# Performance work log

Hardware: AMD Instinct MI355X
Metric: run time of the kernel (lower is better)

Reference implementation:

```python
import jax, jax.numpy as jnp
import numpy as np
from jax import lax

S = 2          # scale_factor
K = 5          # k_reassembly
KK = K * K     # 25 reassembly weights per output pixel


def _conv2d(x, w, b, pad):
    y = lax.conv_general_dilated(x, w, (1, 1), [(pad, pad), (pad, pad)],
                                 dimension_numbers=('NCHW', 'OIHW', 'NCHW'))
    return y + b[None, :, None, None]


def _pixel_shuffle(x, r):
    # (N, C*r*r, H, W) -> (N, C, H*r, W*r), torch PixelShuffle semantics
    n, crr, h, w = x.shape
    c = crr // (r * r)
    x = x.reshape(n, c, r, r, h, w)
    x = x.transpose(0, 1, 4, 2, 5, 3)
    return x.reshape(n, c, h * r, w * r)


def setup_inputs() -> dict:
    key = jax.random.key(0)
    k1, k2, k3 = jax.random.split(key, 3)
    x = jax.random.normal(k1, (4, 256, 64, 64), dtype=jnp.float32)
    w_comp = jax.random.normal(k2, (64, 256, 1, 1), dtype=jnp.float32) * 0.05
    b_comp = jnp.zeros((64,), dtype=jnp.float32)
    w_enc = jax.random.normal(k3, (S * S * KK, 64, 3, 3), dtype=jnp.float32) * 0.05
    b_enc = jnp.zeros((S * S * KK,), dtype=jnp.float32)
    return {"x": x, "w_comp": w_comp, "b_comp": b_comp, "w_enc": w_enc, "b_enc": b_enc}


def reference(x, w_comp, b_comp, w_enc, b_enc):
    N, C, H, W = x.shape
    p = K // 2
    # kernel prediction branch
    compressed = _conv2d(x, w_comp, b_comp, pad=0)                 # (N, 64, H, W)
    kernels = _conv2d(compressed, w_enc, b_enc, pad=1)             # (N, S*S*KK, H, W)
    kernels = _pixel_shuffle(kernels, S)                           # (N, KK, H*S, W*S)
    kernels = jax.nn.softmax(kernels, axis=1)
    # regroup kernels: (N, KK, Hs, Ws) -> (N, H, W, KK, S*S)  (torch unfold order: kh then kw)
    k_unf = kernels.reshape(N, KK, H, S, W, S)
    k_unf = k_unf.transpose(0, 2, 4, 1, 3, 5).reshape(N, H, W, KK, S * S)
    # gather KxK input patches: (N, C, H, W, KK), flattened (ih, iw) with ih outer
    xp = jnp.pad(x, ((0, 0), (0, 0), (p, p), (p, p)))
    patches = jnp.stack([xp[:, :, i:i + H, j:j + W]
                         for i in range(K) for j in range(K)], axis=-1)
    # weighted reassembly: per-pixel (C, KK) @ (KK, S*S)
    out = jnp.einsum('nchwk,nhwkq->nhwcq', patches, k_unf)          # (N, H, W, C, S*S)
    out = out.reshape(N, H, W, C * S * S).transpose(0, 3, 1, 2)     # (N, C*S*S, H, W)
    return _pixel_shuffle(out, S)                                   # (N, C, H*S, W*S)
```

## Files before the change

### kernel.cpp

```cpp
#include <hip/hip_runtime.h>
#include <hip/hip_fp16.h>

#define NB 4
#define CI 256
#define HH 64
#define WW 64
#define MC 64
#define HS 128
#define WS_ 128
#define HW 4096

typedef __attribute__((ext_vector_type(8))) short short8v;
typedef __attribute__((ext_vector_type(4))) float floatx4;

__device__ inline unsigned short f2bf(float f) {
  union { float f; unsigned u; } v; v.f = f;
  unsigned r = v.u + 0x7FFFu + ((v.u >> 16) & 1u);
  return (unsigned short)(r >> 16);
}

__global__ __launch_bounds__(256) void prep_kernel(
    const float* __restrict__ w_comp, const float* __restrict__ w_enc,
    unsigned short* __restrict__ Aw1, unsigned short* __restrict__ Aw2) {
  int i = blockIdx.x * 256 + threadIdx.x;
  if (i < 16384) {
    int kl = i & 31, o = (i >> 5) & 63, ks = i >> 11;
    Aw1[i] = f2bf(w_comp[o * 256 + ks * 32 + kl]);
  } else if (i < 16384 + 64512) {
    int j = i - 16384;
    int kl = j & 31, o = (j >> 5) % 112, ks = (j >> 5) / 112;
    int t = ks >> 1, m = (ks & 1) * 32 + kl;
    Aw2[j] = (o < 100) ? f2bf(w_enc[o * 576 + m * 9 + t]) : (unsigned short)0;
  }
}

__global__ __launch_bounds__(512, 1) void conv1x1_mfma(
    const float* __restrict__ x, const unsigned short* __restrict__ Aw1,
    const float* __restrict__ b_comp, unsigned short* __restrict__ comp_cl) {
  __shared__ float pacc[2][64][49];
  int tid = threadIdx.x;
  int wid = tid >> 6, lane = tid & 63;
  int tileid = wid & 1, kh = wid >> 1;
  int Nt = blockIdx.x * 2 + tileid;
  int n = Nt >> 8, pixbase = (Nt & 255) * 16;
  int l15 = lane & 15, g = lane >> 4;
  int pix = pixbase + l15;

  floatx4 acc[4];
#pragma unroll
  for (int ot = 0; ot < 4; ++ot) acc[ot] = (floatx4){0.f, 0.f, 0.f, 0.f};

  const float* xb = x + (size_t)n * CI * HW + pix;
  const unsigned short* ab = Aw1 + l15 * 32 + g * 8;

#pragma unroll
  for (int s = 0; s < 2; ++s) {
    int ks = kh * 2 + s;
    int c0 = ks * 32 + g * 8;
    short8v bfrag;
#pragma unroll
    for (int j = 0; j < 8; ++j)
      bfrag[j] = (short)f2bf(xb[(size_t)(c0 + j) * HW]);
#pragma unroll
    for (int ot = 0; ot < 4; ++ot) {
      short8v af = *(const short8v*)(ab + (ks * 64 + ot * 16) * 32);
      acc[ot] = __builtin_amdgcn_mfma_f32_16x16x32_bf16(af, bfrag, acc[ot], 0, 0, 0);
    }
  }

  if (kh > 0) {
#pragma unroll
    for (int ot = 0; ot < 4; ++ot)
#pragma unroll
      for (int r = 0; r < 4; ++r)
        pacc[tileid][lane][(kh - 1) * 16 + ot * 4 + r] = acc[ot][r];
  }
  __syncthreads();
  if (kh == 0) {
    unsigned short* cp = comp_cl + ((size_t)(n * HW + pix)) * 64;
#pragma unroll
    for (int ot = 0; ot < 4; ++ot) {
      const float4 bv = *(const float4*)(b_comp + ot * 16 + g * 4);
      float v0 = acc[ot][0] + bv.x, v1 = acc[ot][1] + bv.y;
      float v2 = acc[ot][2] + bv.z, v3 = acc[ot][3] + bv.w;
#pragma unroll
      for (int sl = 0; sl < 3; ++sl) {
        v0 += pacc[tileid][lane][sl * 16 + ot * 4 + 0];
        v1 += pacc[tileid][lane][sl * 16 + ot * 4 + 1];
        v2 += pacc[tileid][lane][sl * 16 + ot * 4 + 2];
        v3 += pacc[tileid][lane][sl * 16 + ot * 4 + 3];
      }
      unsigned h01 = (unsigned)f2bf(v0) | ((unsigned)f2bf(v1) << 16);
      unsigned h23 = (unsigned)f2bf(v2) | ((unsigned)f2bf(v3) << 16);
      *(int2*)(cp + ot * 16 + g * 4) = make_int2((int)h01, (int)h23);
    }
  }
}

#define PKLO(W, D, ACC)                                                        \
  asm("v_pk_fma_f16 %0, %1, %2, %0 op_sel:[0,0,0] op_sel_hi:[1,0,1]"           \
      : "+v"(ACC) : "v"(W), "v"(D));
#define PKHI(W, D, ACC)                                                        \
  asm("v_pk_fma_f16 %0, %1, %2, %0 op_sel:[0,1,0] op_sel_hi:[1,1,1]"           \
      : "+v"(ACC) : "v"(W), "v"(D));

#define ROWPK(WA, WB, WC, WD, WE, VA, VB, VC, VD, VE, RP)                      \
  { const unsigned* rr = (const unsigned*)(RP);                                \
    unsigned d0 = rr[0], d1 = rr[1], d2 = rr[2];                               \
    PKLO(WA, d0, aA) PKHI(WB, d0, aA) PKLO(WC, d1, aA)                         \
    PKHI(WD, d1, aA) PKLO(WE, d2, aA)                                          \
    PKHI(VA, d0, aB) PKLO(VB, d1, aB) PKHI(VC, d1, aB)                         \
    PKLO(VD, d2, aB) PKHI(VE, d2, aB) }

__device__ __forceinline__ float4 load_slot20(const float* __restrict__ xb,
                                              int h0, int w0, int f,
                                              bool interior) {
  int c = f / 30, rem = f - c * 30, r = rem / 5, h = rem - r * 5;
  int gh = h0 - 2 + r, gw = w0 - 2 + h * 4;
  if (interior) {
    const float* gp = xb + (size_t)c * HW + gh * WW + gw;
    float2 lo = *(const float2*)gp;
    float2 hi = *(const float2*)(gp + 2);
    return make_float4(lo.x, lo.y, hi.x, hi.y);
  }
  int ghc = min(max(gh, 0), 63);
  const float* rowp = xb + (size_t)c * HW + ghc * WW;
  float v0 = rowp[min(max(gw + 0, 0), 63)];
  float v1 = rowp[min(max(gw + 1, 0), 63)];
  float v2 = rowp[min(max(gw + 2, 0), 63)];
  float v3 = rowp[min(max(gw + 3, 0), 63)];
  bool rok = ((unsigned)gh < 64u);
  v0 = (rok && (unsigned)(gw + 0) < 64u) ? v0 : 0.f;
  v1 = (rok && (unsigned)(gw + 1) < 64u) ? v1 : 0.f;
  v2 = (rok && (unsigned)(gw + 2) < 64u) ? v2 : 0.f;
  v3 = (rok && (unsigned)(gw + 3) < 64u) ? v3 : 0.f;
  return make_float4(v0, v1, v2, v3);
}

__device__ __forceinline__ uint2 f4_to_h4(float4 s) {
  __half2 a = __floats2half2_rn(s.x, s.y);
  __half2 b = __floats2half2_rn(s.z, s.w);
  return make_uint2(*(unsigned*)&a, *(unsigned*)&b);
}

__global__ __launch_bounds__(512, 4) void fused_kernel(
    const float* __restrict__ x,
    const unsigned short* __restrict__ comp_cl,
    const unsigned short* __restrict__ Aw2,
    const float* __restrict__ b_enc,
    float* __restrict__ out) {
  __shared__ float smem[12672];
  float* paccF = smem;
  unsigned short* xph = (unsigned short*)smem;
  unsigned int* wlds = (unsigned int*)(smem + 10880);

  int tid = threadIdx.x;
  int bid = blockIdx.x;
  int tile = bid & 127, n = bid >> 7;
  int tyi = tile >> 2, txi = tile & 3;
  int ty0 = tyi * 4, tx0 = txi * 32;
  int h0 = tyi * 2, w0 = txi * 16;

  int wid = tid >> 6, lane = tid & 63;
  int tileid = wid & 1, kh = wid >> 1;
  int l15 = lane & 15, g = lane >> 4;

  bool interior = (tyi >= 1) && (tyi <= 30) && (txi >= 1) && (txi <= 2);
  bool extra = tid < 448;

  const float* xb0g = x + (size_t)(n * CI) * HW;
  float4 pre0f = load_slot20(xb0g, h0, w0, tid, interior);
  float4 pre1f = extra ? load_slot20(xb0g, h0, w0, tid + 512, interior)
                       : make_float4(0.f, 0.f, 0.f, 0.f);

  {
    int pix = (h0 + tileid) * 64 + w0 + l15;
    int y = pix >> 6, xcol = pix & 63;

    bool vm[9];
    int sh9[9];
#pragma unroll
    for (int t = 0; t < 9; ++t) {
      int dy = t / 3, dx = t % 3;
      vm[t] = ((unsigned)(y + dy - 1) < 64u) && ((unsigned)(xcol + dx - 1) < 64u);
      sh9[t] = (dy - 1) * 64 + (dx - 1);
    }

    floatx4 acc[7];
#pragma unroll
    for (int ot = 0; ot < 7; ++ot) acc[ot] = (floatx4){0.f, 0.f, 0.f, 0.f};

    const unsigned short* cb = comp_cl + (size_t)n * HW * 64;
    const unsigned short* ab = Aw2 + l15 * 32 + g * 8;
    const short8v zv = {0, 0, 0, 0, 0, 0, 0, 0};

    int ks0 = (kh < 2) ? kh * 5 : 10 + (kh - 2) * 4;
    int len = (kh < 2) ? 5 : 4;

    short8v bf[5];
#pragma unroll
    for (int s = 0; s < 5; ++s) {
      int ks = ks0 + s; if (ks > 17) ks = 17;
      int t = ks >> 1, mh = ks & 1;
      const unsigned short* bp = cb + (pix + sh9[t]) * 64 + mh * 32 + g * 8;
      bf[s] = vm[t] ? *(const short8v*)bp : zv;
    }

#pragma unroll
    for (int s = 0; s < 5; ++s) {
      if (s < len) {
        int ks = ks0 + s;
#pragma unroll
        for (int ot = 0; ot < 7; ++ot) {
          short8v af = *(const short8v*)(ab + (ks * 112 + ot * 16) * 32);
          acc[ot] = __builtin_amdgcn_mfma_f32_16x16x32_bf16(af, bf[s], acc[ot], 0, 0, 0);
        }
      }
    }

    if (kh > 0) {
#pragma unroll
      for (int ot = 0; ot < 7; ++ot)
#pragma unroll
        for (int r = 0; r < 4; ++r)
          paccF[(tileid * 64 + lane) * 85 + (kh - 1) * 28 + ot * 4 + r] =
              acc[ot][r];
    }
    __syncthreads();
    if (kh == 0) {
#pragma unroll
      for (int ot = 0; ot < 7; ++ot) {
        int ob = ot * 16 + g * 4; if (ob > 96) ob = 96;
        const float4 bv = *(const float4*)(b_enc + ob);
        acc[ot][0] += bv.x; acc[ot][1] += bv.y;
        acc[ot][2] += bv.z; acc[ot][3] += bv.w;
#pragma unroll
        for (int sl = 0; sl < 3; ++sl) {
          acc[ot][0] += paccF[(tileid * 64 + lane) * 85 + sl * 28 + ot * 4 + 0];
          acc[ot][1] += paccF[(tileid * 64 + lane) * 85 + sl * 28 + ot * 4 + 1];
          acc[ot][2] += paccF[(tileid * 64 + lane) * 85 + sl * 28 + ot * 4 + 2];
          acc[ot][3] += paccF[(tileid * 64 + lane) * 85 + sl * 28 + ot * 4 + 3];
        }
      }

#pragma unroll
      for (int r = 0; r < 4; ++r) {
        float m = acc[0][r];
#pragma unroll
        for (int ot = 1; ot < 6; ++ot) m = fmaxf(m, acc[ot][r]);
        if (g == 0) m = fmaxf(m, acc[6][r]);
        m = fmaxf(m, __shfl_xor(m, 16));
        m = fmaxf(m, __shfl_xor(m, 32));
        float s = 0.f;
        float e[7];
#pragma unroll
        for (int ot = 0; ot < 7; ++ot) {
          bool val = (ot < 6) || (g == 0);
          e[ot] = val ? __expf(acc[ot][r] - m) : 0.f;
          s += e[ot];
        }
        s += __shfl_xor(s, 16);
        s += __shfl_xor(s, 32);
        float inv = 1.f / s;
#pragma unroll
        for (int ot = 0; ot < 7; ++ot) acc[ot][r] = e[ot] * inv;
      }

#pragma unroll
      for (int sh = 0; sh < 2; ++sh) {
        unsigned int* wq = wlds + sh * 896 + tileid * 448 + l15 * 28;
#pragma unroll
        for (int ot = 0; ot < 7; ++ot) {
          if ((ot < 6) || (g == 0)) {
            __half2 h2 = __floats2half2_rn(acc[ot][2 * sh], acc[ot][2 * sh + 1]);
            wq[ot * 4 + g] = *reinterpret_cast<unsigned int*>(&h2);
          }
        }
      }
    }
  }
  __syncthreads();

  int cslot = tid >> 5;
  int rem = tid & 31;
  int py = rem >> 4;
  int shsel = (rem >> 3) & 1;
  int pxp = rem & 7;
  int oy = ty0 + 2 * py + shsel;
  int ox0 = tx0 + 4 * pxp;
  int cb0 = 2 * pxp;

  const unsigned int* wtA = wlds + shsel * 896 + py * 448 + cb0 * 28;
  const unsigned int* wtB = wtA + 28;
  uint4 A0 = *(const uint4*)(wtA + 0);
  uint4 A1 = *(const uint4*)(wtA + 4);
  uint4 A2 = *(const uint4*)(wtA + 8);
  uint4 A3 = *(const uint4*)(wtA + 12);
  uint4 A4 = *(const uint4*)(wtA + 16);
  uint4 A5 = *(const uint4*)(wtA + 20);
  unsigned int A6 = wtA[24];
  uint4 B0 = *(const uint4*)(wtB + 0);
  uint4 B1 = *(const uint4*)(wtB + 4);
  uint4 B2 = *(const uint4*)(wtB + 8);
  uint4 B3 = *(const uint4*)(wtB + 12);
  uint4 B4 = *(const uint4*)(wtB + 16);
  uint4 B5 = *(const uint4*)(wtB + 20);
  unsigned int B6 = wtB[24];

  {
    uint2 p0 = f4_to_h4(pre0f);
    *(uint2*)(xph + 4 * tid) = p0;
    if (extra) {
      uint2 p1 = f4_to_h4(pre1f);
      *(uint2*)(xph + 4 * (tid + 512)) = p1;
    }
  }
  __syncthreads();

  for (int cs = 0; cs < 8; ++cs) {
    unsigned short* xpcur = xph + (cs & 1) * 3840;
    unsigned short* xpnxt = xph + ((cs + 1) & 1) * 3840;

    uint2 t0 = make_uint2(0u, 0u), t1 = make_uint2(0u, 0u);
    if (cs < 7) {
      const float* xbn = x + (size_t)(n * CI + (cs + 1) * 32) * HW;
      t0 = f4_to_h4(load_slot20(xbn, h0, w0, tid, interior));
      if (extra) t1 = f4_to_h4(load_slot20(xbn, h0, w0, tid + 512, interior));
    }

    float* outb = out + ((size_t)(n * CI + cs * 32) * HS + oy) * WS_ + ox0;
#pragma unroll
    for (int it = 0; it < 2; ++it) {
      int cl = it * 16 + cslot;
      const unsigned short* p = xpcur + cl * 120 + py * 20 + cb0;
      unsigned aA = 0u, aB = 0u;
      ROWPK(A0.x, A0.y, A0.z, A0.w, A1.x, B0.x, B0.y, B0.z, B0.w, B1.x, p)
      ROWPK(A1.y, A1.z, A1.w, A2.x, A2.y, B1.y, B1.z, B1.w, B2.x, B2.y, p + 20)
      ROWPK(A2.z, A2.w, A3.x, A3.y, A3.z, B2.z, B2.w, B3.x, B3.y, B3.z, p + 40)
      ROWPK(A3.w, A4.x, A4.y, A4.z, A4.w, B3.w, B4.x, B4.y, B4.z, B4.w, p + 60)
      ROWPK(A5.x, A5.y, A5.z, A5.w, A6,   B5.x, B5.y, B5.z, B5.w, B6,   p + 80)
      __half2 hA = *reinterpret_cast<__half2*>(&aA);
      __half2 hB = *reinterpret_cast<__half2*>(&aB);
      float2 fA = __half22float2(hA);
      float2 fB = __half22float2(hB);
      *(float4*)(outb + (size_t)cl * HS * WS_) =
          make_float4(fA.x, fA.y, fB.x, fB.y);
    }

    if (cs < 7) {
      *(uint2*)(xpnxt + 4 * tid) = t0;
      if (extra) *(uint2*)(xpnxt + 4 * (tid + 512)) = t1;
      __syncthreads();
    }
  }
}

extern "C" void kernel_launch(void* const* d_in, const int* in_sizes, int n_in,
                              void* d_out, int out_size, void* d_ws,
                              size_t ws_size, hipStream_t stream) {
  const float* x      = (const float*)d_in[0];
  const float* w_comp = (const float*)d_in[1];
  const float* b_comp = (const float*)d_in[2];
  const float* w_enc  = (const float*)d_in[3];
  const float* b_enc  = (const float*)d_in[4];
  float* out = (float*)d_out;

  char* ws = (char*)d_ws;
  unsigned short* comp_cl = (unsigned short*)ws;
  unsigned short* Aw1     = (unsigned short*)(ws + 2097152);
  unsigned short* Aw2     = (unsigned short*)(ws + 2129920);

  prep_kernel<<<dim3(316), 256, 0, stream>>>(w_comp, w_enc, Aw1, Aw2);
  conv1x1_mfma<<<dim3(512), 512, 0, stream>>>(x, Aw1, b_comp, comp_cl);
  fused_kernel<<<dim3(512), 512, 0, stream>>>(x, comp_cl, Aw2, b_enc, out);
}
```

Measured before the change: 54.04 us.

## Widen halo to 16B-aligned float4 loads and deepen x prefetch to triple buffer

```diff
diff --git a/kernel.cpp b/kernel.cpp
--- a/kernel.cpp
+++ b/kernel.cpp
@@ -112,16 +112,13 @@
     PKHI(VA, d0, aB) PKLO(VB, d1, aB) PKHI(VC, d1, aB)                         \
     PKLO(VD, d2, aB) PKHI(VE, d2, aB) }
 
-__device__ __forceinline__ float4 load_slot20(const float* __restrict__ xb,
+__device__ __forceinline__ float4 load_slot24(const float* __restrict__ xb,
                                               int h0, int w0, int f,
                                               bool interior) {
-  int c = f / 30, rem = f - c * 30, r = rem / 5, h = rem - r * 5;
-  int gh = h0 - 2 + r, gw = w0 - 2 + h * 4;
+  int c = f / 36, rem = f - c * 36, r = rem / 6, h = rem - r * 6;
+  int gh = h0 - 2 + r, gw = w0 - 4 + h * 4;
   if (interior) {
-    const float* gp = xb + (size_t)c * HW + gh * WW + gw;
-    float2 lo = *(const float2*)gp;
-    float2 hi = *(const float2*)(gp + 2);
-    return make_float4(lo.x, lo.y, hi.x, hi.y);
+    return *(const float4*)(xb + (size_t)c * HW + gh * WW + gw);
   }
   int ghc = min(max(gh, 0), 63);
   const float* rowp = xb + (size_t)c * HW + ghc * WW;
@@ -166,11 +163,12 @@
   int l15 = lane & 15, g = lane >> 4;
 
   bool interior = (tyi >= 1) && (tyi <= 30) && (txi >= 1) && (txi <= 2);
-  bool extra = tid < 448;
+  bool extra3 = tid < 128;
 
   const float* xb0g = x + (size_t)(n * CI) * HW;
-  float4 pre0f = load_slot20(xb0g, h0, w0, tid, interior);
-  float4 pre1f = extra ? load_slot20(xb0g, h0, w0, tid + 512, interior)
+  float4 preA = load_slot24(xb0g, h0, w0, tid, interior);
+  float4 preB = load_slot24(xb0g, h0, w0, tid + 512, interior);
+  float4 preC = extra3 ? load_slot24(xb0g, h0, w0, tid + 1024, interior)
                        : make_float4(0.f, 0.f, 0.f, 0.f);
 
   {
@@ -307,38 +305,44 @@
   uint4 B5 = *(const uint4*)(wtB + 20);
   unsigned int B6 = wtB[24];
 
+  *(uint2*)(xph + 4 * tid) = f4_to_h4(preA);
+  *(uint2*)(xph + 4 * (tid + 512)) = f4_to_h4(preB);
+  if (extra3) *(uint2*)(xph + 4 * (tid + 1024)) = f4_to_h4(preC);
+
+  float4 wA, wB, wC;
   {
-    uint2 p0 = f4_to_h4(pre0f);
-    *(uint2*)(xph + 4 * tid) = p0;
-    if (extra) {
-      uint2 p1 = f4_to_h4(pre1f);
-      *(uint2*)(xph + 4 * (tid + 512)) = p1;
-    }
+    const float* xb1 = x + (size_t)(n * CI + 32) * HW;
+    wA = load_slot24(xb1, h0, w0, tid, interior);
+    wB = load_slot24(xb1, h0, w0, tid + 512, interior);
+    wC = extra3 ? load_slot24(xb1, h0, w0, tid + 1024, interior)
+                : make_float4(0.f, 0.f, 0.f, 0.f);
   }
   __syncthreads();
 
   for (int cs = 0; cs < 8; ++cs) {
-    unsigned short* xpcur = xph + (cs & 1) * 3840;
-    unsigned short* xpnxt = xph + ((cs + 1) & 1) * 3840;
-
-    uint2 t0 = make_uint2(0u, 0u), t1 = make_uint2(0u, 0u);
-    if (cs < 7) {
-      const float* xbn = x + (size_t)(n * CI + (cs + 1) * 32) * HW;
-      t0 = f4_to_h4(load_slot20(xbn, h0, w0, tid, interior));
-      if (extra) t1 = f4_to_h4(load_slot20(xbn, h0, w0, tid + 512, interior));
+    unsigned short* xpcur = xph + (cs % 3) * 4608;
+    unsigned short* xpnxt = xph + ((cs + 1) % 3) * 4608;
+
+    float4 lA = make_float4(0.f, 0.f, 0.f, 0.f);
+    float4 lB = lA, lC = lA;
+    if (cs < 6) {
+      const float* xbn = x + (size_t)(n * CI + (cs + 2) * 32) * HW;
+      lA = load_slot24(xbn, h0, w0, tid, interior);
+      lB = load_slot24(xbn, h0, w0, tid + 512, interior);
+      if (extra3) lC = load_slot24(xbn, h0, w0, tid + 1024, interior);
     }
 
     float* outb = out + ((size_t)(n * CI + cs * 32) * HS + oy) * WS_ + ox0;
 #pragma unroll
     for (int it = 0; it < 2; ++it) {
       int cl = it * 16 + cslot;
-      const unsigned short* p = xpcur + cl * 120 + py * 20 + cb0;
+      const unsigned short* p = xpcur + cl * 144 + py * 24 + cb0 + 2;
       unsigned aA = 0u, aB = 0u;
       ROWPK(A0.x, A0.y, A0.z, A0.w, A1.x, B0.x, B0.y, B0.z, B0.w, B1.x, p)
-      ROWPK(A1.y, A1.z, A1.w, A2.x, A2.y, B1.y, B1.z, B1.w, B2.x, B2.y, p + 20)
-      ROWPK(A2.z, A2.w, A3.x, A3.y, A3.z, B2.z, B2.w, B3.x, B3.y, B3.z, p + 40)
-      ROWPK(A3.w, A4.x, A4.y, A4.z, A4.w, B3.w, B4.x, B4.y, B4.z, B4.w, p + 60)
-      ROWPK(A5.x, A5.y, A5.z, A5.w, A6,   B5.x, B5.y, B5.z, B5.w, B6,   p + 80)
+      ROWPK(A1.y, A1.z, A1.w, A2.x, A2.y, B1.y, B1.z, B1.w, B2.x, B2.y, p + 24)
+      ROWPK(A2.z, A2.w, A3.x, A3.y, A3.z, B2.z, B2.w, B3.x, B3.y, B3.z, p + 48)
+      ROWPK(A3.w, A4.x, A4.y, A4.z, A4.w, B3.w, B4.x, B4.y, B4.z, B4.w, p + 72)
+      ROWPK(A5.x, A5.y, A5.z, A5.w, A6,   B5.x, B5.y, B5.z, B5.w, B6,   p + 96)
       __half2 hA = *reinterpret_cast<__half2*>(&aA);
       __half2 hB = *reinterpret_cast<__half2*>(&aB);
       float2 fA = __half22float2(hA);
@@ -348,10 +352,12 @@
     }
 
     if (cs < 7) {
-      *(uint2*)(xpnxt + 4 * tid) = t0;
-      if (extra) *(uint2*)(xpnxt + 4 * (tid + 512)) = t1;
+      *(uint2*)(xpnxt + 4 * tid) = f4_to_h4(wA);
+      *(uint2*)(xpnxt + 4 * (tid + 512)) = f4_to_h4(wB);
+      if (extra3) *(uint2*)(xpnxt + 4 * (tid + 1024)) = f4_to_h4(wC);
       __syncthreads();
     }
+    wA = lA; wB = lB; wC = lC;
   }
 }
 
```

Measured after the change: 56.70 us. 4.9% more time.
